# Optimization experiments

Measured on AMD Instinct MI355X. Metric: run time of the kernel, lower is better.

The kernel has to match this reference:

```python
import jax, jax.numpy as jnp
import numpy as np

NUM_HEADS = 16
ROTARY_BASE = 10000.0


def _rope_cos_sin(seqlen, rotary_dim, dtype):
    # inv_freq: (rotary_dim/2,), cos/sin: (seqlen, rotary_dim/2)
    inv_freq = 1.0 / (ROTARY_BASE ** (jnp.arange(0, rotary_dim, 2, dtype=jnp.float32) / rotary_dim))
    t = jnp.arange(seqlen, dtype=jnp.float32)
    freqs = jnp.outer(t, inv_freq)
    return jnp.cos(freqs).astype(dtype), jnp.sin(freqs).astype(dtype)


def _apply_rotary(x, cos, sin):
    # x: (b, s, h, d); cos/sin: (s, d/2). Non-interleaved (GPT-NeoX) halves.
    d2 = cos.shape[-1]
    x1, x2 = x[..., :d2], x[..., d2:2 * d2]
    c = cos[None, :, None, :]
    s = sin[None, :, None, :]
    r1 = x1 * c - x2 * s
    r2 = x1 * s + x2 * c
    return jnp.concatenate([r1, r2], axis=-1)


def setup_inputs() -> dict:
    key = jax.random.key(0)
    ks = jax.random.split(key, 5)
    B, S, E = 2, 2048, 2048
    x = jax.random.normal(ks[0], (B, S, E), dtype=jnp.float32)
    wqkv_w = jax.random.normal(ks[1], (3 * E, E), dtype=jnp.float32) * 0.02
    wqkv_b = jax.random.normal(ks[2], (3 * E,), dtype=jnp.float32) * 0.02
    out_w = jax.random.normal(ks[3], (E, E), dtype=jnp.float32) * 0.02
    out_b = jax.random.normal(ks[4], (E,), dtype=jnp.float32) * 0.02
    return {"x": x, "wqkv_w": wqkv_w, "wqkv_b": wqkv_b, "out_w": out_w, "out_b": out_b}


def reference(x, wqkv_w, wqkv_b, out_w, out_b):
    B, S, E = x.shape
    H = NUM_HEADS
    D = E // H
    # fused QKV projection: (b, s, 3, h, d)
    qkv = (jnp.einsum('bse,fe->bsf', x, wqkv_w) + wqkv_b).reshape(B, S, 3, H, D)
    q, k, v = qkv[:, :, 0], qkv[:, :, 1], qkv[:, :, 2]
    # rotary embedding on full head_dim of q and k
    cos, sin = _rope_cos_sin(S, D, x.dtype)
    q = _apply_rotary(q, cos, sin)
    k = _apply_rotary(k, cos, sin)
    # causal self-attention, softmax_scale = 1/sqrt(head_dim)
    scale = 1.0 / jnp.sqrt(jnp.asarray(D, dtype=x.dtype))
    scores = jnp.einsum('bshd,bthd->bhst', q, k) * scale
    causal_mask = jnp.tril(jnp.ones((S, S), dtype=bool))
    scores = jnp.where(causal_mask[None, None], scores, jnp.asarray(-1e30, dtype=scores.dtype))
    attn = jax.nn.softmax(scores, axis=-1)
    ctx = jnp.einsum('bhst,bthd->bshd', attn, v).reshape(B, S, E)
    return jnp.einsum('bse,fe->bsf', ctx, out_w) + out_b
```

## Files before the change

### kernel.cpp

```cpp
#include <hip/hip_runtime.h>

typedef unsigned short u16;
typedef unsigned int u32;
typedef __bf16 bf16x8 __attribute__((ext_vector_type(8)));
typedef float fx4 __attribute__((ext_vector_type(4)));

__device__ __forceinline__ float bf2f(u16 u) {
    return __uint_as_float(((u32)u) << 16);
}
__device__ __forceinline__ u16 f2bf(float f) {
    u32 x = __float_as_uint(f);
    u32 r = (x + 0x7fffu + ((x >> 16) & 1u)) >> 16;
    return (u16)r;
}

__device__ __forceinline__ void gld16(const u16* g, u16* l) {
    __builtin_amdgcn_global_load_lds(
        (const __attribute__((address_space(1))) void*)g,
        (__attribute__((address_space(3))) void*)l, 16, 0, 0);
}

#define MFMA16(a, b, c) __builtin_amdgcn_mfma_f32_16x16x32_bf16((a), (b), (c), 0, 0, 0)

__global__ __launch_bounds__(256) void cvt_kernel(const float* __restrict__ x,
                                                  const float* __restrict__ w1,
                                                  const float* __restrict__ w2,
                                                  u16* __restrict__ xb,
                                                  u16* __restrict__ w1b,
                                                  u16* __restrict__ w2b) {
    size_t g = ((size_t)blockIdx.x * 256 + threadIdx.x) * 8;
    const float* src;
    u16* dst;
    if (g < 8388608) {
        src = x;
        dst = xb;
    } else if (g < 20971520) {
        src = w1 - 8388608;
        dst = w1b - 8388608;
    } else {
        src = w2 - 20971520;
        dst = w2b - 20971520;
    }
    float4 a = *(const float4*)&src[g];
    float4 b = *(const float4*)&src[g + 4];
    u16 v[8];
    v[0] = f2bf(a.x);
    v[1] = f2bf(a.y);
    v[2] = f2bf(a.z);
    v[3] = f2bf(a.w);
    v[4] = f2bf(b.x);
    v[5] = f2bf(b.y);
    v[6] = f2bf(b.z);
    v[7] = f2bf(b.w);
    *(uint4*)&dst[g] = *(const uint4*)v;
}

template <int MODE>
__global__ __launch_bounds__(256, 2) void gemm_bt(const u16* __restrict__ A,
                                                  const u16* __restrict__ B,
                                                  const float* __restrict__ bias,
                                                  float* __restrict__ Cf,
                                                  u16* __restrict__ qb,
                                                  u16* __restrict__ kb,
                                                  u16* __restrict__ vb,
                                                  int N, int K) {
    __shared__ __align__(16) u16 As[2][128 * 32];
    __shared__ __align__(16) u16 Bs[2][128 * 32];

    const int tid = threadIdx.x;
    const int lane = tid & 63;
    const int wave = tid >> 6;
    const int quad = lane >> 4;
    const int m16 = lane & 15;
    const int wm = wave >> 1, wn = wave & 1;
    const int bm = blockIdx.y * 128, bn = blockIdx.x * 128;

    const int r0 = tid >> 2;
    const int u0 = (tid & 3) ^ ((r0 >> 1) & 3);
    const int r1 = (tid + 256) >> 2;
    const int u1 = ((tid + 256) & 3) ^ ((r1 >> 1) & 3);
    const u16* a0 = &A[(size_t)(bm + r0) * K + u0 * 8];
    const u16* a1 = &A[(size_t)(bm + r1) * K + u1 * 8];
    const u16* b0 = &B[(size_t)(bn + r0) * K + u0 * 8];
    const u16* b1 = &B[(size_t)(bn + r1) * K + u1 * 8];

    const int su = (quad ^ ((m16 >> 1) & 3)) * 8;

#define GLDT(kt_, buf_)                                                       \
    {                                                                         \
        const int k0_ = (kt_) << 5;                                           \
        gld16(a0 + k0_, &As[buf_][tid * 8]);                                  \
        gld16(a1 + k0_, &As[buf_][(tid + 256) * 8]);                          \
        gld16(b0 + k0_, &Bs[buf_][tid * 8]);                                  \
        gld16(b1 + k0_, &Bs[buf_][(tid + 256) * 8]);                          \
    }

    const fx4 zero4 = {0.f, 0.f, 0.f, 0.f};
    fx4 acc[4][4];
#pragma unroll
    for (int i = 0; i < 4; ++i)
#pragma unroll
        for (int j = 0; j < 4; ++j) acc[i][j] = zero4;

    const int nk = K >> 5;
    GLDT(0, 0);
    if (nk > 1) {
        GLDT(1, 1);
        asm volatile("s_waitcnt vmcnt(4)" ::: "memory");
    } else {
        asm volatile("s_waitcnt vmcnt(0)" ::: "memory");
    }
    __builtin_amdgcn_s_barrier();

    int cur = 0;
    for (int kt = 0; kt < nk; ++kt) {
        bf16x8 af[4], bfr[4];
#pragma unroll
        for (int t = 0; t < 4; ++t) {
            af[t] = *(const bf16x8*)&As[cur][(wm * 64 + t * 16 + m16) * 32 + su];
            bfr[t] = *(const bf16x8*)&Bs[cur][(wn * 64 + t * 16 + m16) * 32 + su];
        }
        __builtin_amdgcn_s_setprio(1);
#pragma unroll
        for (int mt = 0; mt < 4; ++mt)
#pragma unroll
            for (int nt = 0; nt < 4; ++nt)
                acc[mt][nt] = MFMA16(af[mt], bfr[nt], acc[mt][nt]);
        __builtin_amdgcn_s_setprio(0);
        __builtin_amdgcn_sched_barrier(0);
        asm volatile("s_waitcnt lgkmcnt(0)" ::: "memory");
        __builtin_amdgcn_s_barrier();

        if (kt + 2 < nk) {
            GLDT(kt + 2, cur);
            asm volatile("s_waitcnt vmcnt(4)" ::: "memory");
        } else {
            asm volatile("s_waitcnt vmcnt(0)" ::: "memory");
        }
        __builtin_amdgcn_s_barrier();
        cur ^= 1;
    }

#pragma unroll
    for (int mt = 0; mt < 4; ++mt) {
#pragma unroll
        for (int r = 0; r < 4; ++r) {
            int row = bm + wm * 64 + mt * 16 + quad * 4 + r;
#pragma unroll
            for (int nt = 0; nt < 4; ++nt) {
                int col = bn + wn * 64 + nt * 16 + m16;
                float v = acc[mt][nt][r] + bias[col];
                if (MODE == 0) {
                    Cf[(size_t)row * N + col] = v;
                } else {
                    int which = col >> 11;
                    int h = (col >> 7) & 15;
                    int d = col & 127;
                    int b = row >> 11;
                    int s = row & 2047;
                    u16* dst = (which == 0) ? qb : ((which == 1) ? kb : vb);
                    dst[(size_t)((b * 16 + h) * 2048 + s) * 128 + d] = f2bf(v);
                }
            }
        }
    }
}

__global__ __launch_bounds__(256) void rope_kernel(u16* __restrict__ q,
                                                   u16* __restrict__ k) {
    int t = blockIdx.x * 256 + threadIdx.x;
    int i = t & 63;
    int s = (t >> 6) & 2047;
    int bh = t >> 17;
    float inv = exp2f(-(float)i * 0.2076205059304595f);
    float ang = (float)s * inv;
    float sn, cs;
    sincosf(ang, &sn, &cs);
    size_t base = ((size_t)bh * 2048 + s) * 128 + i;
    {
        float x1 = bf2f(q[base]), x2 = bf2f(q[base + 64]);
        q[base] = f2bf(x1 * cs - x2 * sn);
        q[base + 64] = f2bf(x1 * sn + x2 * cs);
    }
    {
        float x1 = bf2f(k[base]), x2 = bf2f(k[base + 64]);
        k[base] = f2bf(x1 * cs - x2 * sn);
        k[base + 64] = f2bf(x1 * sn + x2 * cs);
    }
}

__global__ __launch_bounds__(256) void vtrans_kernel(const u16* __restrict__ v,
                                                     u16* __restrict__ vt) {
    __shared__ __align__(16) u16 L[128 * 66];
    const int tid = threadIdx.x;
    const int kb = blockIdx.x * 64;
    const int bh = blockIdx.y;
    const u16* vp = v + (size_t)bh * 2048 * 128;
    u16* op = vt + (size_t)bh * 128 * 2048;
#pragma unroll
    for (int i = 0; i < 4; ++i) {
        int c = i * 256 + tid;
        int t = c >> 4, d8 = (c & 15) << 3;
        uint4 x = *(const uint4*)&vp[(kb + t) * 128 + d8];
        const u16* xs = (const u16*)&x;
#pragma unroll
        for (int j = 0; j < 8; ++j) L[(d8 + j) * 66 + t] = xs[j];
    }
    __syncthreads();
#pragma unroll
    for (int i = 0; i < 4; ++i) {
        int c = i * 256 + tid;
        int d = c >> 3, t8 = (c & 7) << 3;
        uint4 x;
        u16* xs = (u16*)&x;
#pragma unroll
        for (int j = 0; j < 8; ++j) xs[j] = L[d * 66 + t8 + j];
        *(uint4*)&op[(size_t)d * 2048 + kb + t8] = x;
    }
}

__global__ __launch_bounds__(256, 2) void attn_kernel(const u16* __restrict__ q,
                                                      const u16* __restrict__ k,
                                                      const u16* __restrict__ vt,
                                                      u16* __restrict__ ctx) {
    __shared__ __align__(16) u16 Ks[2][64 * 128];
    __shared__ __align__(16) u16 Vs[2][128 * 64];
    __shared__ __align__(16) u16 Ps[4][16 * 64];

    const int tid = threadIdx.x;
    const int lane = tid & 63;
    const int wave = tid >> 6;
    const int quad = lane >> 4;
    const int m16 = lane & 15;

    const int l = blockIdx.x;
    const int half0 = l & 1;
    const int qt0 = (l >> 1) & 7;
    const int bh = l >> 4;
    const int b = bh >> 4, h = bh & 15;
    const u16* qp = q + (size_t)bh * 2048 * 128;
    const u16* kp = k + (size_t)bh * 2048 * 128;
    const u16* vp = vt + (size_t)bh * 128 * 2048;
    const float scale = 0.08838834764831845f;
    const fx4 zero4 = {0.f, 0.f, 0.f, 0.f};

    int ksrc[4], vsrc[4];
#pragma unroll
    for (int i = 0; i < 4; ++i) {
        int s = tid + i * 256;
        int r = s >> 4, p = s & 15;
        ksrc[i] = r * 128 + (p ^ (r & 7)) * 8;
        int d = s >> 3, pv = s & 7;
        vsrc[i] = d * 2048 + (pv ^ (d & 7)) * 8;
    }

#define GLD_TILE(kb_, buf_)                                                   \
    {                                                                         \
        _Pragma("unroll") for (int ii = 0; ii < 4; ++ii) {                    \
            gld16(kp + (size_t)(kb_)*128 + ksrc[ii],                          \
                  &Ks[buf_][tid * 8 + ii * 2048]);                            \
            gld16(vp + (kb_) + vsrc[ii], &Vs[buf_][tid * 8 + ii * 2048]);     \
        }                                                                     \
    }

#pragma unroll 1
    for (int pass = 0; pass < 2; ++pass) {
        const int qt = pass ? (15 - qt0) : qt0;
        const int hf = pass ? (1 - half0) : half0;
        const int qrow0 = qt * 128 + hf * 64 + wave * 16;
        const int nkt = 2 * qt + 1 + hf;

        bf16x8 qf[4];
#pragma unroll
        for (int c = 0; c < 4; ++c)
            qf[c] = *(const bf16x8*)&qp[(size_t)(qrow0 + m16) * 128 + c * 32 +
                                        quad * 8];

        fx4 o[8];
#pragma unroll
        for (int dn = 0; dn < 8; ++dn) o[dn] = zero4;
        float mi[4], li[4];
#pragma unroll
        for (int r = 0; r < 4; ++r) {
            mi[r] = -1e30f;
            li[r] = 0.f;
        }

        GLD_TILE(0, 0);
        __syncthreads();
        int cur = 0;
        for (int kt = 0; kt < nkt; ++kt) {
            const int kb = kt * 64;
            if (kt + 1 < nkt) GLD_TILE(kb + 64, cur ^ 1);

            fx4 sc[4];
#pragma unroll
            for (int nt = 0; nt < 4; ++nt) sc[nt] = zero4;
            __builtin_amdgcn_s_setprio(1);
#pragma unroll
            for (int c = 0; c < 4; ++c)
#pragma unroll
                for (int nt = 0; nt < 4; ++nt) {
                    int e = (nt * 16 + m16) * 128 + c * 32 + quad * 8;
                    bf16x8 kf =
                        *(const bf16x8*)&Ks[cur][e ^ ((m16 & 7) << 3)];
                    sc[nt] = MFMA16(qf[c], kf, sc[nt]);
                }
            __builtin_amdgcn_s_setprio(0);

#pragma unroll
            for (int r = 0; r < 4; ++r) {
                int rg = qrow0 + quad * 4 + r;
                float mx = mi[r];
#pragma unroll
                for (int nt = 0; nt < 4; ++nt) {
                    int cg = kb + nt * 16 + m16;
                    float s = sc[nt][r] * scale;
                    s = (cg <= rg) ? s : -1e30f;
                    sc[nt][r] = s;
                    mx = fmaxf(mx, s);
                }
                mx = fmaxf(mx, __shfl_xor(mx, 1));
                mx = fmaxf(mx, __shfl_xor(mx, 2));
                mx = fmaxf(mx, __shfl_xor(mx, 4));
                mx = fmaxf(mx, __shfl_xor(mx, 8));
                float alpha = __expf(mi[r] - mx);
                mi[r] = mx;
                float rsum = 0.f;
                int row = quad * 4 + r;
#pragma unroll
                for (int nt = 0; nt < 4; ++nt) {
                    float p = __expf(sc[nt][r] - mx);
                    Ps[wave][(row * 64 + nt * 16 + m16) ^ ((row & 7) << 3)] =
                        f2bf(p);
                    rsum += p;
                }
                rsum += __shfl_xor(rsum, 1);
                rsum += __shfl_xor(rsum, 2);
                rsum += __shfl_xor(rsum, 4);
                rsum += __shfl_xor(rsum, 8);
                li[r] = li[r] * alpha + rsum;
#pragma unroll
                for (int dn = 0; dn < 8; ++dn) o[dn][r] *= alpha;
            }

            __builtin_amdgcn_s_setprio(1);
#pragma unroll
            for (int c2 = 0; c2 < 2; ++c2) {
                bf16x8 pf = *(const bf16x8*)&Ps[wave][(m16 * 64 + c2 * 32 +
                                                       quad * 8) ^
                                                      ((m16 & 7) << 3)];
#pragma unroll
                for (int dn = 0; dn < 8; ++dn) {
                    int e = (dn * 16 + m16) * 64 + c2 * 32 + quad * 8;
                    bf16x8 vf =
                        *(const bf16x8*)&Vs[cur][e ^ ((m16 & 7) << 3)];
                    o[dn] = MFMA16(pf, vf, o[dn]);
                }
            }
            __builtin_amdgcn_s_setprio(0);

            __syncthreads();
            cur ^= 1;
        }

#pragma unroll
        for (int r = 0; r < 4; ++r) {
            int row = qrow0 + quad * 4 + r;
            float inv = 1.0f / li[r];
#pragma unroll
            for (int dn = 0; dn < 8; ++dn) {
                int d = dn * 16 + m16;
                ctx[((size_t)(b * 2048 + row)) * 2048 + h * 128 + d] =
                    f2bf(o[dn][r] * inv);
            }
        }
    }
}

extern "C" void kernel_launch(void* const* d_in, const int* in_sizes, int n_in,
                              void* d_out, int out_size, void* d_ws,
                              size_t ws_size, hipStream_t stream) {
    const float* x = (const float*)d_in[0];
    const float* wqkv_w = (const float*)d_in[1];
    const float* wqkv_b = (const float*)d_in[2];
    const float* out_w = (const float*)d_in[3];
    const float* out_b = (const float*)d_in[4];
    u16* ws = (u16*)d_ws;

    u16* xb = ws;
    u16* wqkvb = ws + 8388608;
    u16* vb = ws + 20971520;
    u16* outwb = ws + 29360128;
    u16* vtb = xb;
    u16* ctx = vb;
    u16* qb = (u16*)d_out;
    u16* kb = qb + 8388608;

    cvt_kernel<<<12288, 256, 0, stream>>>(x, wqkv_w, out_w, xb, wqkvb, outwb);
    gemm_bt<1><<<dim3(48, 32), 256, 0, stream>>>(xb, wqkvb, wqkv_b, nullptr,
                                                 qb, kb, vb, 6144, 2048);
    rope_kernel<<<16384, 256, 0, stream>>>(qb, kb);
    vtrans_kernel<<<dim3(32, 32), 256, 0, stream>>>(vb, vtb);
    attn_kernel<<<512, 256, 0, stream>>>(qb, kb, vtb, ctx);
    gemm_bt<0><<<dim3(16, 32), 256, 0, stream>>>(ctx, outwb, out_b,
                                                 (float*)d_out, nullptr,
                                                 nullptr, nullptr, 2048, 2048);
}
```

Measured before the change: 415.0 us.

## Use dedicated 256x256-tile QKV GEMM kernel with 512 threads and 64-wide K steps

Replaces the generic 128x128 QKV projection GEMM with a dedicated kernel using 256x256 output tiles, 8 waves, and K steps of 64. Each block covers two column passes, so the grid is 192 blocks, matching a one-wave launch over the CUs. Fragment loads are interleaved with MFMA groups to hide LDS latency. The larger tile raises arithmetic intensity per loaded byte, but it uses 128KB of LDS per block and many accumulator registers, which may limit occupancy.

Result: slower. 428.6 us (+3.3%).

```diff
diff --git a/kernel.cpp b/kernel.cpp
--- a/kernel.cpp
+++ b/kernel.cpp
@@ -55,104 +55,155 @@
     *(uint4*)&dst[g] = *(const uint4*)v;
 }
 
-template <int MODE>
-__global__ __launch_bounds__(256, 2) void gemm_bt(const u16* __restrict__ A,
-                                                  const u16* __restrict__ B,
-                                                  const float* __restrict__ bias,
-                                                  float* __restrict__ Cf,
-                                                  u16* __restrict__ qb,
-                                                  u16* __restrict__ kb,
-                                                  u16* __restrict__ vb,
-                                                  int N, int K) {
-    __shared__ __align__(16) u16 As[2][128 * 32];
-    __shared__ __align__(16) u16 Bs[2][128 * 32];
+__global__ __launch_bounds__(512, 2) void gemm_qkv(const u16* __restrict__ A,
+                                                   const u16* __restrict__ B,
+                                                   const float* __restrict__ bias,
+                                                   u16* __restrict__ qb,
+                                                   u16* __restrict__ kb,
+                                                   u16* __restrict__ vb) {
+    const int K = 2048;
+    __shared__ __align__(16) u16 As[2][256 * 64];
+    __shared__ __align__(16) u16 Bs[2][256 * 64];
 
     const int tid = threadIdx.x;
     const int lane = tid & 63;
     const int wave = tid >> 6;
     const int quad = lane >> 4;
     const int m16 = lane & 15;
-    const int wm = wave >> 1, wn = wave & 1;
-    const int bm = blockIdx.y * 128, bn = blockIdx.x * 128;
-
-    const int r0 = tid >> 2;
-    const int u0 = (tid & 3) ^ ((r0 >> 1) & 3);
-    const int r1 = (tid + 256) >> 2;
-    const int u1 = ((tid + 256) & 3) ^ ((r1 >> 1) & 3);
-    const u16* a0 = &A[(size_t)(bm + r0) * K + u0 * 8];
-    const u16* a1 = &A[(size_t)(bm + r1) * K + u1 * 8];
-    const u16* b0 = &B[(size_t)(bn + r0) * K + u0 * 8];
-    const u16* b1 = &B[(size_t)(bn + r1) * K + u1 * 8];
-
-    const int su = (quad ^ ((m16 >> 1) & 3)) * 8;
-
-#define GLDT(kt_, buf_)                                                       \
+    const int wm = wave >> 2, wn = wave & 3;
+
+    const int l = blockIdx.x;
+    const int bm = (l / 12) * 256;
+    const int bn0 = (l % 12) * 256;
+
+    int srow[4], suoff[4];
+#pragma unroll
+    for (int ii = 0; ii < 4; ++ii) {
+        int s = tid + ii * 512;
+        int r = s >> 3, p = s & 7;
+        srow[ii] = r;
+        suoff[ii] = (p ^ (r & 7)) * 8;
+    }
+
+    const int sw = m16 & 7;
+#define LDA_(buf_, rowi_, s_) \
+    (*(const bf16x8*)&As[buf_][(rowi_) * 64 + (((s_)*4 + quad) ^ sw) * 8])
+#define LDB_(buf_, rowi_, s_) \
+    (*(const bf16x8*)&Bs[buf_][(rowi_) * 64 + (((s_)*4 + quad) ^ sw) * 8])
+
+#pragma unroll 1
+    for (int pass = 0; pass < 2; ++pass) {
+        const int bn = bn0 + pass * 3072;
+        const u16* Ab = A + (size_t)bm * K;
+        const u16* Bb = B + (size_t)bn * K;
+
+#define GLDT(k0_, buf_)                                                       \
     {                                                                         \
-        const int k0_ = (kt_) << 5;                                           \
-        gld16(a0 + k0_, &As[buf_][tid * 8]);                                  \
-        gld16(a1 + k0_, &As[buf_][(tid + 256) * 8]);                          \
-        gld16(b0 + k0_, &Bs[buf_][tid * 8]);                                  \
-        gld16(b1 + k0_, &Bs[buf_][(tid + 256) * 8]);                          \
-    }
-
-    const fx4 zero4 = {0.f, 0.f, 0.f, 0.f};
-    fx4 acc[4][4];
-#pragma unroll
-    for (int i = 0; i < 4; ++i)
-#pragma unroll
-        for (int j = 0; j < 4; ++j) acc[i][j] = zero4;
-
-    const int nk = K >> 5;
-    GLDT(0, 0);
-    if (nk > 1) {
-        GLDT(1, 1);
-        asm volatile("s_waitcnt vmcnt(4)" ::: "memory");
-    } else {
-        asm volatile("s_waitcnt vmcnt(0)" ::: "memory");
-    }
-    __builtin_amdgcn_s_barrier();
-
-    int cur = 0;
-    for (int kt = 0; kt < nk; ++kt) {
-        bf16x8 af[4], bfr[4];
-#pragma unroll
-        for (int t = 0; t < 4; ++t) {
-            af[t] = *(const bf16x8*)&As[cur][(wm * 64 + t * 16 + m16) * 32 + su];
-            bfr[t] = *(const bf16x8*)&Bs[cur][(wn * 64 + t * 16 + m16) * 32 + su];
-        }
-        __builtin_amdgcn_s_setprio(1);
-#pragma unroll
-        for (int mt = 0; mt < 4; ++mt)
-#pragma unroll
-            for (int nt = 0; nt < 4; ++nt)
-                acc[mt][nt] = MFMA16(af[mt], bfr[nt], acc[mt][nt]);
-        __builtin_amdgcn_s_setprio(0);
-        __builtin_amdgcn_sched_barrier(0);
-        asm volatile("s_waitcnt lgkmcnt(0)" ::: "memory");
+        _Pragma("unroll") for (int ii = 0; ii < 4; ++ii) {                    \
+            gld16(Ab + (size_t)srow[ii] * K + (k0_) + suoff[ii],              \
+                  &As[buf_][(tid + ii * 512) * 8]);                           \
+            gld16(Bb + (size_t)srow[ii] * K + (k0_) + suoff[ii],              \
+                  &Bs[buf_][(tid + ii * 512) * 8]);                           \
+        }                                                                     \
+    }
+
+        const fx4 zero4 = {0.f, 0.f, 0.f, 0.f};
+        fx4 acc[8][4];
+#pragma unroll
+        for (int i = 0; i < 8; ++i)
+#pragma unroll
+            for (int j = 0; j < 4; ++j) acc[i][j] = zero4;
+
+        const int nk = K >> 6;
+        GLDT(0, 0);
+        GLDT(64, 1);
+        asm volatile("s_waitcnt vmcnt(8)" ::: "memory");
         __builtin_amdgcn_s_barrier();
 
-        if (kt + 2 < nk) {
-            GLDT(kt + 2, cur);
-            asm volatile("s_waitcnt vmcnt(4)" ::: "memory");
-        } else {
-            asm volatile("s_waitcnt vmcnt(0)" ::: "memory");
-        }
-        __builtin_amdgcn_s_barrier();
-        cur ^= 1;
-    }
-
-#pragma unroll
-    for (int mt = 0; mt < 4; ++mt) {
-#pragma unroll
-        for (int r = 0; r < 4; ++r) {
-            int row = bm + wm * 64 + mt * 16 + quad * 4 + r;
-#pragma unroll
-            for (int nt = 0; nt < 4; ++nt) {
-                int col = bn + wn * 64 + nt * 16 + m16;
-                float v = acc[mt][nt][r] + bias[col];
-                if (MODE == 0) {
-                    Cf[(size_t)row * N + col] = v;
-                } else {
+        int cur = 0;
+        for (int kt = 0; kt < nk; ++kt) {
+            const int ar0 = wm * 128 + m16;
+            const int br0 = wn * 64 + m16;
+            bf16x8 afr[4][2], bf01[2][2], bf23[2][2];
+
+#pragma unroll
+            for (int r = 0; r < 4; ++r)
+#pragma unroll
+                for (int s = 0; s < 2; ++s)
+                    afr[r][s] = LDA_(cur, ar0 + r * 16, s);
+#pragma unroll
+            for (int c = 0; c < 2; ++c)
+#pragma unroll
+                for (int s = 0; s < 2; ++s)
+                    bf01[c][s] = LDB_(cur, br0 + c * 16, s);
+            __builtin_amdgcn_s_setprio(1);
+#pragma unroll
+            for (int r = 0; r < 4; ++r)
+#pragma unroll
+                for (int c = 0; c < 2; ++c)
+#pragma unroll
+                    for (int s = 0; s < 2; ++s)
+                        acc[r][c] = MFMA16(afr[r][s], bf01[c][s], acc[r][c]);
+            __builtin_amdgcn_s_setprio(0);
+
+#pragma unroll
+            for (int c = 0; c < 2; ++c)
+#pragma unroll
+                for (int s = 0; s < 2; ++s)
+                    bf23[c][s] = LDB_(cur, br0 + (c + 2) * 16, s);
+            __builtin_amdgcn_s_setprio(1);
+#pragma unroll
+            for (int r = 0; r < 4; ++r)
+#pragma unroll
+                for (int c = 0; c < 2; ++c)
+#pragma unroll
+                    for (int s = 0; s < 2; ++s)
+                        acc[r][c + 2] =
+                            MFMA16(afr[r][s], bf23[c][s], acc[r][c + 2]);
+            __builtin_amdgcn_s_setprio(0);
+
+#pragma unroll
+            for (int r = 0; r < 4; ++r)
+#pragma unroll
+                for (int s = 0; s < 2; ++s)
+                    afr[r][s] = LDA_(cur, ar0 + (r + 4) * 16, s);
+            __builtin_amdgcn_s_setprio(1);
+#pragma unroll
+            for (int r = 0; r < 4; ++r)
+#pragma unroll
+                for (int c = 0; c < 2; ++c)
+#pragma unroll
+                    for (int s = 0; s < 2; ++s) {
+                        acc[r + 4][c + 2] =
+                            MFMA16(afr[r][s], bf23[c][s], acc[r + 4][c + 2]);
+                        acc[r + 4][c] =
+                            MFMA16(afr[r][s], bf01[c][s], acc[r + 4][c]);
+                    }
+            __builtin_amdgcn_s_setprio(0);
+
+            __builtin_amdgcn_sched_barrier(0);
+            asm volatile("s_waitcnt lgkmcnt(0)" ::: "memory");
+            __builtin_amdgcn_s_barrier();
+
+            if (kt + 2 < nk) {
+                GLDT((kt + 2) << 6, cur);
+                asm volatile("s_waitcnt vmcnt(8)" ::: "memory");
+            } else {
+                asm volatile("s_waitcnt vmcnt(0)" ::: "memory");
+            }
+            __builtin_amdgcn_s_barrier();
+            cur ^= 1;
+        }
+
+#pragma unroll
+        for (int mt = 0; mt < 8; ++mt) {
+#pragma unroll
+            for (int rr = 0; rr < 4; ++rr) {
+                int row = bm + wm * 128 + mt * 16 + quad * 4 + rr;
+#pragma unroll
+                for (int nt = 0; nt < 4; ++nt) {
+                    int col = bn + wn * 64 + nt * 16 + m16;
+                    float v = acc[mt][nt][rr] + bias[col];
                     int which = col >> 11;
                     int h = (col >> 7) & 15;
                     int d = col & 127;
@@ -164,6 +215,105 @@
             }
         }
     }
+#undef GLDT
+}
+
+template <int MODE>
+__global__ __launch_bounds__(256, 2) void gemm_bt(const u16* __restrict__ A,
+                                                  const u16* __restrict__ B,
+                                                  const float* __restrict__ bias,
+                                                  float* __restrict__ Cf,
+                                                  int N, int K) {
+    __shared__ __align__(16) u16 As[2][128 * 32];
+    __shared__ __align__(16) u16 Bs[2][128 * 32];
+
+    const int tid = threadIdx.x;
+    const int lane = tid & 63;
+    const int wave = tid >> 6;
+    const int quad = lane >> 4;
+    const int m16 = lane & 15;
+    const int wm = wave >> 1, wn = wave & 1;
+    const int bm = blockIdx.y * 128, bn = blockIdx.x * 128;
+
+    const int r0 = tid >> 2;
+    const int u0 = (tid & 3) ^ ((r0 >> 1) & 3);
+    const int r1 = (tid + 256) >> 2;
+    const int u1 = ((tid + 256) & 3) ^ ((r1 >> 1) & 3);
+    const u16* a0 = &A[(size_t)(bm + r0) * K + u0 * 8];
+    const u16* a1 = &A[(size_t)(bm + r1) * K + u1 * 8];
+    const u16* b0 = &B[(size_t)(bn + r0) * K + u0 * 8];
+    const u16* b1 = &B[(size_t)(bn + r1) * K + u1 * 8];
+
+    const int su = (quad ^ ((m16 >> 1) & 3)) * 8;
+
+#define GLDT(kt_, buf_)                                                       \
+    {                                                                         \
+        const int k0_ = (kt_) << 5;                                           \
+        gld16(a0 + k0_, &As[buf_][tid * 8]);                                  \
+        gld16(a1 + k0_, &As[buf_][(tid + 256) * 8]);                          \
+        gld16(b0 + k0_, &Bs[buf_][tid * 8]);                                  \
+        gld16(b1 + k0_, &Bs[buf_][(tid + 256) * 8]);                          \
+    }
+
+    const fx4 zero4 = {0.f, 0.f, 0.f, 0.f};
+    fx4 acc[4][4];
+#pragma unroll
+    for (int i = 0; i < 4; ++i)
+#pragma unroll
+        for (int j = 0; j < 4; ++j) acc[i][j] = zero4;
+
+    const int nk = K >> 5;
+    GLDT(0, 0);
+    if (nk > 1) {
+        GLDT(1, 1);
+        asm volatile("s_waitcnt vmcnt(4)" ::: "memory");
+    } else {
+        asm volatile("s_waitcnt vmcnt(0)" ::: "memory");
+    }
+    __builtin_amdgcn_s_barrier();
+
+    int cur = 0;
+    for (int kt = 0; kt < nk; ++kt) {
+        bf16x8 af[4], bfr[4];
+#pragma unroll
+        for (int t = 0; t < 4; ++t) {
+            af[t] = *(const bf16x8*)&As[cur][(wm * 64 + t * 16 + m16) * 32 + su];
+            bfr[t] = *(const bf16x8*)&Bs[cur][(wn * 64 + t * 16 + m16) * 32 + su];
+        }
+        __builtin_amdgcn_s_setprio(1);
+#pragma unroll
+        for (int mt = 0; mt < 4; ++mt)
+#pragma unroll
+            for (int nt = 0; nt < 4; ++nt)
+                acc[mt][nt] = MFMA16(af[mt], bfr[nt], acc[mt][nt]);
+        __builtin_amdgcn_s_setprio(0);
+        __builtin_amdgcn_sched_barrier(0);
+        asm volatile("s_waitcnt lgkmcnt(0)" ::: "memory");
+        __builtin_amdgcn_s_barrier();
+
+        if (kt + 2 < nk) {
+            GLDT(kt + 2, cur);
+            asm volatile("s_waitcnt vmcnt(4)" ::: "memory");
+        } else {
+            asm volatile("s_waitcnt vmcnt(0)" ::: "memory");
+        }
+        __builtin_amdgcn_s_barrier();
+        cur ^= 1;
+    }
+
+#pragma unroll
+    for (int mt = 0; mt < 4; ++mt) {
+#pragma unroll
+        for (int r = 0; r < 4; ++r) {
+            int row = bm + wm * 64 + mt * 16 + quad * 4 + r;
+#pragma unroll
+            for (int nt = 0; nt < 4; ++nt) {
+                int col = bn + wn * 64 + nt * 16 + m16;
+                Cf[(size_t)row * N + col] = acc[mt][nt][r] + bias[col];
+            }
+        }
+    }
+#undef GLDT
 }
 
 __global__ __launch_bounds__(256) void rope_kernel(u16* __restrict__ q,
@@ -398,12 +548,10 @@
     u16* kb = qb + 8388608;
 
     cvt_kernel<<<12288, 256, 0, stream>>>(x, wqkv_w, out_w, xb, wqkvb, outwb);
-    gemm_bt<1><<<dim3(48, 32), 256, 0, stream>>>(xb, wqkvb, wqkv_b, nullptr,
-                                                 qb, kb, vb, 6144, 2048);
+    gemm_qkv<<<192, 512, 0, stream>>>(xb, wqkvb, wqkv_b, qb, kb, vb);
     rope_kernel<<<16384, 256, 0, stream>>>(qb, kb);
     vtrans_kernel<<<dim3(32, 32), 256, 0, stream>>>(vb, vtb);
     attn_kernel<<<512, 256, 0, stream>>>(qb, kb, vtb, ctx);
     gemm_bt<0><<<dim3(16, 32), 256, 0, stream>>>(ctx, outwb, out_b,
-                                                 (float*)d_out, nullptr,
-                                                 nullptr, nullptr, 2048, 2048);
-}
+                                                 (float*)d_out, 2048, 2048);
+}
```
